# Kernel tuning notes

Measured on AMD Instinct MI355X. Metric: run time of the kernel, lower is better.

## Reference

```python
import jax, jax.numpy as jnp
import numpy as np

N_NODES = 50000
N_EDGES = 800000
IN_FEATS = 256
OUT_FEATS = 64
NUM_HEADS = 4
EDGE_FEATS = 64
NUM_ETYPES = 8
NEG_SLOPE = 0.2


def setup_inputs() -> dict:
    key = jax.random.key(0)
    ks = jax.random.split(key, 10)
    feat = jax.random.normal(ks[0], (N_NODES, IN_FEATS), dtype=jnp.float32)
    e_feat = jax.random.randint(ks[1], (N_EDGES,), 0, NUM_ETYPES)
    src = jax.random.randint(ks[2], (N_EDGES,), 0, N_NODES)
    dst = jax.random.randint(ks[3], (N_EDGES,), 0, N_NODES)
    # parameters (xavier-normal-ish scale)
    W_fc = jax.random.normal(ks[4], (IN_FEATS, NUM_HEADS * OUT_FEATS), dtype=jnp.float32) * 0.05
    W_e = jax.random.normal(ks[5], (EDGE_FEATS, NUM_HEADS * EDGE_FEATS), dtype=jnp.float32) * 0.1
    edge_emb = jax.random.normal(ks[6], (NUM_ETYPES, EDGE_FEATS), dtype=jnp.float32)
    attn_l = jax.random.normal(ks[7], (NUM_HEADS, OUT_FEATS), dtype=jnp.float32) * 0.1
    attn_r = jax.random.normal(ks[8], (NUM_HEADS, OUT_FEATS), dtype=jnp.float32) * 0.1
    attn_e = jax.random.normal(ks[9], (NUM_HEADS, EDGE_FEATS), dtype=jnp.float32) * 0.1
    return {"feat": feat, "e_feat": e_feat, "src": src, "dst": dst,
            "W_fc": W_fc, "W_e": W_e, "edge_emb": edge_emb,
            "attn_l": attn_l, "attn_r": attn_r, "attn_e": attn_e}


def reference(feat, e_feat, src, dst, W_fc, W_e, edge_emb, attn_l, attn_r, attn_e):
    N = feat.shape[0]
    H, D = attn_l.shape
    # node projection: [N, H, D]
    ft = (feat @ W_fc).reshape(N, H, D)
    # edge-type embedding -> per-head edge feature: [E, H, edge_feats]
    ef = (edge_emb[e_feat] @ W_e).reshape(-1, H, attn_e.shape[1])
    ee = jnp.einsum('ehf,hf->eh', ef, attn_e)          # [E, H]
    el = jnp.einsum('nhd,hd->nh', ft, attn_l)          # [N, H]
    er = jnp.einsum('nhd,hd->nh', ft, attn_r)          # [N, H]
    # edge logits: u_add_v + edge-type term, leaky relu
    e = el[src] + er[dst] + ee                          # [E, H]
    e = jnp.where(e > 0, e, NEG_SLOPE * e)
    # segment softmax grouped by destination node
    m = jax.ops.segment_max(e, dst, num_segments=N)     # [N, H]
    ex = jnp.exp(e - m[dst])
    s = jax.ops.segment_sum(ex, dst, num_segments=N)    # [N, H]
    a = ex / s[dst]                                     # [E, H]
    # weighted scatter-sum aggregation: sum_e ft[src_e] * a_e -> dst_e
    rst = jax.ops.segment_sum(ft[src] * a[:, :, None], dst, num_segments=N)  # [N, H, D]
    return rst, a
```

## Files before the change

kernel.cpp:

```cpp
#include <hip/hip_runtime.h>

#define H 4
#define D 64
#define C 256
#define IN_F 256
#define EF 64
#define NEG 0.2f

typedef unsigned short ushort_t;
typedef __attribute__((ext_vector_type(8))) short bf16x8;
typedef __attribute__((ext_vector_type(4))) float f32x4;

__device__ __forceinline__ ushort_t f2bf(float x) {
    unsigned u = __float_as_uint(x);
    unsigned r = u + 0x7FFFu + ((u >> 16) & 1u);
    return (ushort_t)(r >> 16);
}

__global__ void k_misc(const float* __restrict__ W, ushort_t* __restrict__ WT,
                       const float* __restrict__ edge_emb, const float* __restrict__ W_e,
                       const float* __restrict__ attn_e, float* __restrict__ ee) {
    int b = blockIdx.x;
    if (b < 16) {
        __shared__ float tile[64][65];
        int bi = b >> 2, bj = b & 3;
        int lane = threadIdx.x & 63, wv = threadIdx.x >> 6;
        #pragma unroll
        for (int i = 0; i < 16; ++i) {
            int row = wv * 16 + i;
            tile[row][lane] = W[(size_t)(bi * 64 + row) * 256 + bj * 64 + lane];
        }
        __syncthreads();
        #pragma unroll
        for (int i = 0; i < 16; ++i) {
            int row = wv * 16 + i;
            WT[(size_t)(bj * 64 + row) * 256 + bi * 64 + lane] = f2bf(tile[lane][row]);
        }
    } else {
        int t = b - 16;
        int c = threadIdx.x;
        float acc = 0.f;
        #pragma unroll 8
        for (int k = 0; k < EF; ++k)
            acc += edge_emb[t * EF + k] * W_e[k * C + c];
        acc *= attn_e[c];
        #pragma unroll
        for (int s = 32; s > 0; s >>= 1) acc += __shfl_down(acc, s, 64);
        if ((threadIdx.x & 63) == 0) ee[t * H + (threadIdx.x >> 6)] = acc;
    }
}

#define BM 128
#define BK 64
__launch_bounds__(512)
__global__ void k_gemm(const float* __restrict__ feat, const ushort_t* __restrict__ Bbf,
                       const float* __restrict__ attn_l, const float* __restrict__ attn_r,
                       ushort_t* __restrict__ ftbf, float* __restrict__ el, float* __restrict__ er,
                       int N) {
    __shared__ ushort_t As[BM * BK];
    __shared__ ushort_t Bs[C * BK];
    int t = threadIdx.x;
    int l = t & 63, w = t >> 6;
    int wr = w >> 2, wc = w & 3;
    int m0 = blockIdx.x * BM;

    f32x4 zero = {0.f, 0.f, 0.f, 0.f};
    f32x4 acc[4][4];
    #pragma unroll
    for (int i = 0; i < 4; ++i)
        #pragma unroll
        for (int j = 0; j < 4; ++j) acc[i][j] = zero;

    for (int ks = 0; ks < 4; ++ks) {
        #pragma unroll
        for (int i = 0; i < 2; ++i) {
            int c   = t + i * 512;
            int row = c >> 3;
            int kg  = c & 7;
            int kgs = kg ^ (row & 7);
            int gr = m0 + row;
            float4 a0 = {0.f,0.f,0.f,0.f}, a1 = {0.f,0.f,0.f,0.f};
            if (gr < N) {
                const float* ap = feat + (size_t)gr * 256 + ks * BK + kg * 8;
                a0 = *(const float4*)ap;
                a1 = *(const float4*)(ap + 4);
            }
            ushort_t v[8];
            v[0]=f2bf(a0.x); v[1]=f2bf(a0.y); v[2]=f2bf(a0.z); v[3]=f2bf(a0.w);
            v[4]=f2bf(a1.x); v[5]=f2bf(a1.y); v[6]=f2bf(a1.z); v[7]=f2bf(a1.w);
            *(uint4*)(&As[row * BK + kgs * 8]) = *(uint4*)v;
        }
        #pragma unroll
        for (int i = 0; i < 4; ++i) {
            int c   = t + i * 512;
            int row = c >> 3;
            int kg  = c & 7;
            int kgs = kg ^ (row & 7);
            *(uint4*)(&Bs[row * BK + kgs * 8]) =
                *(const uint4*)(Bbf + (size_t)row * 256 + ks * BK + kg * 8);
        }
        __syncthreads();
        #pragma unroll
        for (int k2 = 0; k2 < 2; ++k2) {
            bf16x8 av[4], bv[4];
            int kc = (l >> 4) + k2 * 4;
            #pragma unroll
            for (int i = 0; i < 4; ++i) {
                int ra = wr * 64 + i * 16 + (l & 15);
                av[i] = *(const bf16x8*)(&As[ra * BK + (kc ^ (ra & 7)) * 8]);
                int rb = wc * 64 + i * 16 + (l & 15);
                bv[i] = *(const bf16x8*)(&Bs[rb * BK + (kc ^ (rb & 7)) * 8]);
            }
            #pragma unroll
            for (int i = 0; i < 4; ++i)
                #pragma unroll
                for (int j = 0; j < 4; ++j)
                    acc[i][j] = __builtin_amdgcn_mfma_f32_16x16x32_bf16(av[i], bv[j], acc[i][j], 0, 0, 0);
        }
        __syncthreads();
    }

    int cb = wc * 64;
    int h  = wc;
    float wl[4], wrg[4];
    #pragma unroll
    for (int j = 0; j < 4; ++j) {
        int d = j * 16 + (l & 15);
        wl[j]  = attn_l[h * 64 + d];
        wrg[j] = attn_r[h * 64 + d];
    }
    int rbase = m0 + wr * 64;
    #pragma unroll
    for (int i = 0; i < 4; ++i) {
        #pragma unroll
        for (int r = 0; r < 4; ++r) {
            int m = rbase + i * 16 + (l >> 4) * 4 + r;
            float pl = 0.f, pr = 0.f;
            #pragma unroll
            for (int j = 0; j < 4; ++j) {
                float v = acc[i][j][r];
                ftbf[(size_t)m * 256 + cb + j * 16 + (l & 15)] = f2bf(v);
                pl = fmaf(v, wl[j], pl);
                pr = fmaf(v, wrg[j], pr);
            }
            #pragma unroll
            for (int s2 = 1; s2 <= 8; s2 <<= 1) {
                pl += __shfl_xor(pl, s2, 64);
                pr += __shfl_xor(pr, s2, 64);
            }
            if ((l & 15) == 0 && m < N) { el[m * H + h] = pl; er[m * H + h] = pr; }
        }
    }
}

__global__ void k_deg(const int* __restrict__ dst, unsigned* __restrict__ deg, int E) {
    int i = (blockIdx.x * 256 + threadIdx.x) * 4;
    if (i + 3 < E) {
        int4 d = *(const int4*)(dst + i);
        atomicAdd(&deg[d.x], 1u); atomicAdd(&deg[d.y], 1u);
        atomicAdd(&deg[d.z], 1u); atomicAdd(&deg[d.w], 1u);
    } else {
        for (int k = 0; k < 4; ++k)
            if (i + k < E) atomicAdd(&deg[dst[i + k]], 1u);
    }
}

__global__ void k_scan(const unsigned* __restrict__ deg, unsigned* __restrict__ off,
                       unsigned* __restrict__ cursor, int n) {
    __shared__ unsigned wsum[16];
    __shared__ unsigned carry_s;
    int t = threadIdx.x;
    int lane = t & 63, wv = t >> 6;
    if (t == 0) carry_s = 0;
    __syncthreads();
    int ns = n + 1;
    int ntile = (ns + 4095) >> 12;
    for (int tile = 0; tile < ntile; ++tile) {
        int i0 = (tile << 12) + t * 4;
        uint4 v;
        if (i0 + 3 < n) {
            v = *(const uint4*)(deg + i0);
        } else {
            v.x = (i0 + 0 < n) ? deg[i0 + 0] : 0u;
            v.y = (i0 + 1 < n) ? deg[i0 + 1] : 0u;
            v.z = (i0 + 2 < n) ? deg[i0 + 2] : 0u;
            v.w = (i0 + 3 < n) ? deg[i0 + 3] : 0u;
        }
        unsigned s = v.x + v.y + v.z + v.w;
        unsigned sc = s;
        #pragma unroll
        for (int d = 1; d < 64; d <<= 1) {
            unsigned u = __shfl_up(sc, d, 64);
            if (lane >= d) sc += u;
        }
        if (lane == 63) wsum[wv] = sc;
        __syncthreads();
        unsigned carry = carry_s;
        unsigned woff = 0;
        #pragma unroll
        for (int k = 0; k < 16; ++k) woff += (k < wv) ? wsum[k] : 0u;
        unsigned ex0 = carry + woff + sc - s;
        uint4 o;
        o.x = ex0; o.y = ex0 + v.x; o.z = o.y + v.y; o.w = o.z + v.z;
        *(uint4*)(off + i0) = o;
        *(uint4*)(cursor + i0) = o;
        __syncthreads();
        if (t == 1023) carry_s = carry + woff + sc;
    }
}

__global__ void k_scatlog(const int* __restrict__ dst, const int* __restrict__ src,
                          const int* __restrict__ efeat,
                          unsigned* __restrict__ cursor,
                          const float4* __restrict__ el4, const float4* __restrict__ er4,
                          const float4* __restrict__ ee4,
                          float4* __restrict__ exq, uint2* __restrict__ es, int E) {
    int e = blockIdx.x * 256 + threadIdx.x;
    if (e >= E) return;
    int d = dst[e], s = src[e];
    unsigned q = atomicAdd(&cursor[d], 1u);
    float4 l = el4[s];
    float4 r = er4[d];
    float4 te = ee4[efeat[e]];
    float4 v;
    v.x = l.x + r.x + te.x; v.y = l.y + r.y + te.y;
    v.z = l.z + r.z + te.z; v.w = l.w + r.w + te.w;
    v.x = v.x > 0.f ? v.x : NEG * v.x;
    v.y = v.y > 0.f ? v.y : NEG * v.y;
    v.z = v.z > 0.f ? v.z : NEG * v.z;
    v.w = v.w > 0.f ? v.w : NEG * v.w;
    v.x = __expf(v.x); v.y = __expf(v.y); v.z = __expf(v.z); v.w = __expf(v.w);
    exq[q] = v;
    es[q] = make_uint2((unsigned)e, (unsigned)s);
}

__device__ __forceinline__ void macc8(float* acc, uint4 f, float a) {
    unsigned u[4] = {f.x, f.y, f.z, f.w};
    #pragma unroll
    for (int q = 0; q < 4; ++q) {
        float lo = __uint_as_float(u[q] << 16);
        float hi = __uint_as_float(u[q] & 0xFFFF0000u);
        acc[2*q]   = fmaf(lo, a, acc[2*q]);
        acc[2*q+1] = fmaf(hi, a, acc[2*q+1]);
    }
}

__launch_bounds__(256)
__global__ void k_agg(const unsigned* __restrict__ off, const uint2* __restrict__ es,
                      const float* __restrict__ exs, const ushort_t* __restrict__ ft,
                      float4* __restrict__ out4, float* __restrict__ out_a, int N) {
    int node = (int)((blockIdx.x * (size_t)blockDim.x + threadIdx.x) >> 6);
    if (node >= N) return;
    int lane = threadIdx.x & 63;
    unsigned beg = off[node], end = off[node + 1];

    int h1 = lane >> 4, i16 = lane & 15;
    float s = 0.f;
    for (unsigned j = beg + i16; j < end; j += 16)
        s += exs[j * 4 + h1];
    #pragma unroll
    for (int m = 1; m <= 8; m <<= 1) s += __shfl_xor(s, m, 64);
    float inv_h = (end > beg) ? 1.f / s : 0.f;

    int g  = lane >> 4;
    int li = lane & 15;
    int h2 = li >> 2;
    float inv2 = __shfl(inv_h, h2 * 16, 64);
    float inva = __shfl(inv_h, (lane & 3) * 16, 64);

    float acc[16];
    #pragma unroll
    for (int q = 0; q < 16; ++q) acc[q] = 0.f;

    unsigned j = beg;
    for (; j + 3 < end; j += 4) {
        unsigned jj = j + g;
        uint2 e2 = es[jj];
        float a  = exs[jj * 4 + h2] * inv2;
        float aw = exs[jj * 4 + (lane & 3)];
        const ushort_t* fp = ft + (size_t)e2.y * 256 + li * 16;
        uint4 f0 = *(const uint4*)fp;
        uint4 f1 = *(const uint4*)(fp + 8);
        macc8(acc, f0, a);
        macc8(acc + 8, f1, a);
        if (li < 4) out_a[e2.x * 4 + li] = aw * inva;
    }
    if (j < end) {
        unsigned jj = j + g;
        bool act = jj < end;
        unsigned jc = act ? jj : beg;
        uint2 e2 = es[jc];
        float a = act ? exs[jc * 4 + h2] * inv2 : 0.f;
        const ushort_t* fp = ft + (size_t)e2.y * 256 + li * 16;
        uint4 f0 = *(const uint4*)fp;
        uint4 f1 = *(const uint4*)(fp + 8);
        macc8(acc, f0, a);
        macc8(acc + 8, f1, a);
        if (act && li < 4) out_a[e2.x * 4 + li] = exs[jc * 4 + li] * inva;
    }

    #pragma unroll
    for (int q = 0; q < 16; ++q) {
        acc[q] += __shfl_xor(acc[q], 16, 64);
        acc[q] += __shfl_xor(acc[q], 32, 64);
    }
    if (g == 0) {
        #pragma unroll
        for (int k = 0; k < 4; ++k) {
            float4 o = {acc[k*4], acc[k*4+1], acc[k*4+2], acc[k*4+3]};
            out4[(size_t)node * 64 + li * 4 + k] = o;
        }
    }
}

extern "C" void kernel_launch(void* const* d_in, const int* in_sizes, int n_in,
                              void* d_out, int out_size, void* d_ws, size_t ws_size,
                              hipStream_t stream) {
    const float* feat     = (const float*)d_in[0];
    const int*   e_feat   = (const int*)d_in[1];
    const int*   src      = (const int*)d_in[2];
    const int*   dst      = (const int*)d_in[3];
    const float* W_fc     = (const float*)d_in[4];
    const float* W_e      = (const float*)d_in[5];
    const float* edge_emb = (const float*)d_in[6];
    const float* attn_l   = (const float*)d_in[7];
    const float* attn_r   = (const float*)d_in[8];
    const float* attn_e   = (const float*)d_in[9];

    int N = in_sizes[0] / IN_F;
    int E = in_sizes[1];
    int Mpad   = ((N + BM - 1) / BM) * BM;
    int offpad = (((N + 1) + 4095) >> 12) << 12;
    int Epad2  = (E + 1) & ~1;

    float* out_rst = (float*)d_out;
    float* out_a   = out_rst + (size_t)N * C;

    ushort_t* WTbf = (ushort_t*)d_ws;
    ushort_t* ftbf = WTbf + 256 * 256;
    float* el = (float*)(ftbf + (size_t)Mpad * 256);
    float* er = el + (size_t)N * H;
    float* ee = er + (size_t)N * H;
    unsigned* deg    = (unsigned*)(ee + 64);
    unsigned* off    = deg + offpad;
    unsigned* cursor = off + offpad;
    uint2*    es     = (uint2*)(cursor + offpad);
    float4*   exq    = (float4*)(es + Epad2);

    hipMemsetAsync(deg, 0, (size_t)offpad * sizeof(unsigned), stream);

    k_misc   <<<24, 256, 0, stream>>>(W_fc, WTbf, edge_emb, W_e, attn_e, ee);
    k_deg    <<<(E / 4 + 255) / 256, 256, 0, stream>>>(dst, deg, E);
    k_scan   <<<1, 1024, 0, stream>>>(deg, off, cursor, N);
    k_gemm   <<<Mpad / BM, 512, 0, stream>>>(feat, WTbf, attn_l, attn_r, ftbf, el, er, N);
    k_scatlog<<<(E + 255) / 256, 256, 0, stream>>>(dst, src, e_feat, cursor,
                                                   (const float4*)el, (const float4*)er,
                                                   (const float4*)ee, exq, es, E);
    k_agg    <<<((size_t)N * 64 + 255) / 256, 256, 0, stream>>>(off, es, (const float*)exq,
                                                                ftbf, (float4*)out_rst, out_a, N);
}
```

Measured before the change: 309.8 us.

## Pack edge records, move alpha output to coalesced per-edge kernel, fuse degree count

```diff
diff --git a/kernel.cpp b/kernel.cpp
--- a/kernel.cpp
+++ b/kernel.cpp
@@ -11,15 +11,18 @@
 typedef __attribute__((ext_vector_type(8))) short bf16x8;
 typedef __attribute__((ext_vector_type(4))) float f32x4;
 
+struct __align__(32) Rec { float4 ex; unsigned src; unsigned pad[3]; };
+
 __device__ __forceinline__ ushort_t f2bf(float x) {
     unsigned u = __float_as_uint(x);
     unsigned r = u + 0x7FFFu + ((u >> 16) & 1u);
     return (ushort_t)(r >> 16);
 }
 
-__global__ void k_misc(const float* __restrict__ W, ushort_t* __restrict__ WT,
-                       const float* __restrict__ edge_emb, const float* __restrict__ W_e,
-                       const float* __restrict__ attn_e, float* __restrict__ ee) {
+__global__ void k_front(const float* __restrict__ W, ushort_t* __restrict__ WT,
+                        const float* __restrict__ edge_emb, const float* __restrict__ W_e,
+                        const float* __restrict__ attn_e, float* __restrict__ ee,
+                        const int* __restrict__ dst, unsigned* __restrict__ deg, int E) {
     int b = blockIdx.x;
     if (b < 16) {
         __shared__ float tile[64][65];
@@ -36,7 +39,7 @@
             int row = wv * 16 + i;
             WT[(size_t)(bj * 64 + row) * 256 + bi * 64 + lane] = f2bf(tile[lane][row]);
         }
-    } else {
+    } else if (b < 24) {
         int t = b - 16;
         int c = threadIdx.x;
         float acc = 0.f;
@@ -47,6 +50,16 @@
         #pragma unroll
         for (int s = 32; s > 0; s >>= 1) acc += __shfl_down(acc, s, 64);
         if ((threadIdx.x & 63) == 0) ee[t * H + (threadIdx.x >> 6)] = acc;
+    } else {
+        int i = ((b - 24) * 256 + threadIdx.x) * 4;
+        if (i + 3 < E) {
+            int4 d = *(const int4*)(dst + i);
+            atomicAdd(&deg[d.x], 1u); atomicAdd(&deg[d.y], 1u);
+            atomicAdd(&deg[d.z], 1u); atomicAdd(&deg[d.w], 1u);
+        } else {
+            for (int k = 0; k < 4; ++k)
+                if (i + k < E) atomicAdd(&deg[dst[i + k]], 1u);
+        }
     }
 }
 
@@ -150,18 +163,6 @@
             }
             if ((l & 15) == 0 && m < N) { el[m * H + h] = pl; er[m * H + h] = pr; }
         }
-    }
-}
-
-__global__ void k_deg(const int* __restrict__ dst, unsigned* __restrict__ deg, int E) {
-    int i = (blockIdx.x * 256 + threadIdx.x) * 4;
-    if (i + 3 < E) {
-        int4 d = *(const int4*)(dst + i);
-        atomicAdd(&deg[d.x], 1u); atomicAdd(&deg[d.y], 1u);
-        atomicAdd(&deg[d.z], 1u); atomicAdd(&deg[d.w], 1u);
-    } else {
-        for (int k = 0; k < 4; ++k)
-            if (i + k < E) atomicAdd(&deg[dst[i + k]], 1u);
     }
 }
 
@@ -214,7 +215,7 @@
                           unsigned* __restrict__ cursor,
                           const float4* __restrict__ el4, const float4* __restrict__ er4,
                           const float4* __restrict__ ee4,
-                          float4* __restrict__ exq, uint2* __restrict__ es, int E) {
+                          Rec* __restrict__ recs, int E) {
     int e = blockIdx.x * 256 + threadIdx.x;
     if (e >= E) return;
     int d = dst[e], s = src[e];
@@ -230,8 +231,9 @@
     v.z = v.z > 0.f ? v.z : NEG * v.z;
     v.w = v.w > 0.f ? v.w : NEG * v.w;
     v.x = __expf(v.x); v.y = __expf(v.y); v.z = __expf(v.z); v.w = __expf(v.w);
-    exq[q] = v;
-    es[q] = make_uint2((unsigned)e, (unsigned)s);
+    Rec* rp = &recs[q];
+    rp->ex = v;
+    rp->src = (unsigned)s;
 }
 
 __device__ __forceinline__ void macc8(float* acc, uint4 f, float a) {
@@ -246,27 +248,31 @@
 }
 
 __launch_bounds__(256)
-__global__ void k_agg(const unsigned* __restrict__ off, const uint2* __restrict__ es,
-                      const float* __restrict__ exs, const ushort_t* __restrict__ ft,
-                      float4* __restrict__ out4, float* __restrict__ out_a, int N) {
+__global__ void k_agg(const unsigned* __restrict__ off, const Rec* __restrict__ recs,
+                      const ushort_t* __restrict__ ft, float4* __restrict__ out4,
+                      float4* __restrict__ invs, int N) {
     int node = (int)((blockIdx.x * (size_t)blockDim.x + threadIdx.x) >> 6);
     if (node >= N) return;
     int lane = threadIdx.x & 63;
     unsigned beg = off[node], end = off[node + 1];
+    const float* rf = (const float*)recs;
 
     int h1 = lane >> 4, i16 = lane & 15;
     float s = 0.f;
     for (unsigned j = beg + i16; j < end; j += 16)
-        s += exs[j * 4 + h1];
+        s += rf[(size_t)j * 8 + h1];
     #pragma unroll
     for (int m = 1; m <= 8; m <<= 1) s += __shfl_xor(s, m, 64);
     float inv_h = (end > beg) ? 1.f / s : 0.f;
+
+    float i0 = __shfl(inv_h, 0, 64),  i1 = __shfl(inv_h, 16, 64),
+          i2 = __shfl(inv_h, 32, 64), i3 = __shfl(inv_h, 48, 64);
+    if (lane == 0) invs[node] = make_float4(i0, i1, i2, i3);
 
     int g  = lane >> 4;
     int li = lane & 15;
     int h2 = li >> 2;
-    float inv2 = __shfl(inv_h, h2 * 16, 64);
-    float inva = __shfl(inv_h, (lane & 3) * 16, 64);
+    float inv2 = (h2 == 0) ? i0 : (h2 == 1) ? i1 : (h2 == 2) ? i2 : i3;
 
     float acc[16];
     #pragma unroll
@@ -275,28 +281,25 @@
     unsigned j = beg;
     for (; j + 3 < end; j += 4) {
         unsigned jj = j + g;
-        uint2 e2 = es[jj];
-        float a  = exs[jj * 4 + h2] * inv2;
-        float aw = exs[jj * 4 + (lane & 3)];
-        const ushort_t* fp = ft + (size_t)e2.y * 256 + li * 16;
+        float a = rf[(size_t)jj * 8 + h2] * inv2;
+        unsigned sn = ((const unsigned*)recs)[(size_t)jj * 8 + 4];
+        const ushort_t* fp = ft + (size_t)sn * 256 + li * 16;
         uint4 f0 = *(const uint4*)fp;
         uint4 f1 = *(const uint4*)(fp + 8);
         macc8(acc, f0, a);
         macc8(acc + 8, f1, a);
-        if (li < 4) out_a[e2.x * 4 + li] = aw * inva;
     }
     if (j < end) {
         unsigned jj = j + g;
         bool act = jj < end;
         unsigned jc = act ? jj : beg;
-        uint2 e2 = es[jc];
-        float a = act ? exs[jc * 4 + h2] * inv2 : 0.f;
-        const ushort_t* fp = ft + (size_t)e2.y * 256 + li * 16;
+        float a = act ? rf[(size_t)jc * 8 + h2] * inv2 : 0.f;
+        unsigned sn = ((const unsigned*)recs)[(size_t)jc * 8 + 4];
+        const ushort_t* fp = ft + (size_t)sn * 256 + li * 16;
         uint4 f0 = *(const uint4*)fp;
         uint4 f1 = *(const uint4*)(fp + 8);
         macc8(acc, f0, a);
         macc8(acc + 8, f1, a);
-        if (act && li < 4) out_a[e2.x * 4 + li] = exs[jc * 4 + li] * inva;
     }
 
     #pragma unroll
@@ -311,6 +314,30 @@
             out4[(size_t)node * 64 + li * 4 + k] = o;
         }
     }
+}
+
+__global__ void k_alpha(const int* __restrict__ dst, const int* __restrict__ src,
+                        const int* __restrict__ efeat,
+                        const float4* __restrict__ el4, const float4* __restrict__ er4,
+                        const float4* __restrict__ ee4, const float4* __restrict__ invs,
+                        float4* __restrict__ out_a4, int E) {
+    int e = blockIdx.x * 256 + threadIdx.x;
+    if (e >= E) return;
+    int d = dst[e], s = src[e];
+    float4 l = el4[s];
+    float4 r = er4[d];
+    float4 te = ee4[efeat[e]];
+    float4 v;
+    v.x = l.x + r.x + te.x; v.y = l.y + r.y + te.y;
+    v.z = l.z + r.z + te.z; v.w = l.w + r.w + te.w;
+    v.x = v.x > 0.f ? v.x : NEG * v.x;
+    v.y = v.y > 0.f ? v.y : NEG * v.y;
+    v.z = v.z > 0.f ? v.z : NEG * v.z;
+    v.w = v.w > 0.f ? v.w : NEG * v.w;
+    v.x = __expf(v.x); v.y = __expf(v.y); v.z = __expf(v.z); v.w = __expf(v.w);
+    float4 iv = invs[d];
+    v.x *= iv.x; v.y *= iv.y; v.z *= iv.z; v.w *= iv.w;
+    out_a4[e] = v;
 }
 
 extern "C" void kernel_launch(void* const* d_in, const int* in_sizes, int n_in,
@@ -331,7 +358,6 @@
     int E = in_sizes[1];
     int Mpad   = ((N + BM - 1) / BM) * BM;
     int offpad = (((N + 1) + 4095) >> 12) << 12;
-    int Epad2  = (E + 1) & ~1;
 
     float* out_rst = (float*)d_out;
     float* out_a   = out_rst + (size_t)N * C;
@@ -341,21 +367,27 @@
     float* el = (float*)(ftbf + (size_t)Mpad * 256);
     float* er = el + (size_t)N * H;
     float* ee = er + (size_t)N * H;
-    unsigned* deg    = (unsigned*)(ee + 64);
+    float* invs = ee + 64;
+    unsigned* deg    = (unsigned*)(invs + (size_t)N * H);
     unsigned* off    = deg + offpad;
     unsigned* cursor = off + offpad;
-    uint2*    es     = (uint2*)(cursor + offpad);
-    float4*   exq    = (float4*)(es + Epad2);
+    Rec* recs        = (Rec*)(cursor + offpad);
 
     hipMemsetAsync(deg, 0, (size_t)offpad * sizeof(unsigned), stream);
 
-    k_misc   <<<24, 256, 0, stream>>>(W_fc, WTbf, edge_emb, W_e, attn_e, ee);
-    k_deg    <<<(E / 4 + 255) / 256, 256, 0, stream>>>(dst, deg, E);
+    int degblocks = (E / 4 + 255) / 256;
+    k_front  <<<24 + degblocks, 256, 0, stream>>>(W_fc, WTbf, edge_emb, W_e, attn_e, ee,
+                                                  dst, deg, E);
     k_scan   <<<1, 1024, 0, stream>>>(deg, off, cursor, N);
     k_gemm   <<<Mpad / BM, 512, 0, stream>>>(feat, WTbf, attn_l, attn_r, ftbf, el, er, N);
     k_scatlog<<<(E + 255) / 256, 256, 0, stream>>>(dst, src, e_feat, cursor,
                                                    (const float4*)el, (const float4*)er,
-                                                   (const float4*)ee, exq, es, E);
-    k_agg    <<<((size_t)N * 64 + 255) / 256, 256, 0, stream>>>(off, es, (const float*)exq,
-                                                                ftbf, (float4*)out_rst, out_a, N);
-}
+                                                   (const float4*)ee, recs, E);
+    k_agg    <<<((size_t)N * 64 + 255) / 256, 256, 0, stream>>>(off, recs, ftbf,
+                                                                (float4*)out_rst,
+                                                                (float4*)invs, N);
+    k_alpha  <<<(E + 255) / 256, 256, 0, stream>>>(dst, src, e_feat,
+                                                   (const float4*)el, (const float4*)er,
+                                                   (const float4*)ee, (const float4*)invs,
+                                                   (float4*)out_a, E);
+}
```

Measured after the change: 308.0 us. Within noise of the previous version (-0.6%).
